# Performance work log

Hardware: AMD Instinct MI355X
Metric: run time of the kernel (lower is better)

## Reference

```python
import jax, jax.numpy as jnp
import numpy as np

N_NODES = 100000
N_REL = 8
N_EDGES = 1_600_000
ED = 64   # entity_dim
RD = 64   # relation_dim
H = 4     # attention heads
A = 16    # attention dim per head
D1, D2 = 32, 16  # conv_dim_list


def _leaky(x):
    return jax.nn.leaky_relu(x, 0.01)  # nn.LeakyReLU default slope


def _l2norm(x):
    n = jnp.sqrt(jnp.sum(x * x, axis=1, keepdims=True))
    return x / jnp.maximum(n, 1e-12)  # F.normalize(p=2, dim=1)


def setup_inputs() -> dict:
    key = jax.random.key(0)
    ks = jax.random.split(key, 16)
    s = 0.1
    return dict(
        src=jax.random.randint(ks[0], (N_EDGES,), 0, N_NODES),
        dst=jax.random.randint(ks[1], (N_EDGES,), 0, N_NODES),
        etype=jax.random.randint(ks[2], (N_EDGES,), 0, N_REL),
        node_ids=jnp.arange(N_NODES),
        user_ids=jax.random.randint(ks[3], (1000,), 0, N_NODES),
        item_ids=jax.random.randint(ks[4], (4096,), 0, N_NODES),
        entity_embed=jax.random.normal(ks[5], (N_NODES, ED)) * s,
        rel_embed=jax.random.normal(ks[6], (N_REL, RD)) * s,
        W_R=jax.random.normal(ks[7], (N_REL, ED, RD)) * s,
        W_A=jax.random.normal(ks[8], (RD, H, A)) * s,
        W1_0=jax.random.normal(ks[9], (ED, D1 // H)) * s,
        b1_0=jnp.zeros((D1 // H,)),
        W2_0=jax.random.normal(ks[10], (ED, D1 // H)) * s,
        b2_0=jnp.zeros((D1 // H,)),
        W1_1=jax.random.normal(ks[11], (D1, D2 // H)) * s,
        b1_1=jnp.zeros((D2 // H,)),
        W2_1=jax.random.normal(ks[12], (D1, D2 // H)) * s,
        b2_1=jnp.zeros((D2 // H,)),
    )


def _compute_attention(entity_embed, rel_embed, W_R, W_A, src, dst, etype):
    # relation-specific edge attention: tanh(e_src W_r W_A) * tanh(e_dst W_r W_A + r W_A)
    WA_flat = W_A.reshape(RD, H * A)
    W_ra = jnp.einsum('rij,jk->rik', W_R, WA_flat)          # [R, ED, H*A]
    proj = jnp.einsum('ne,rek->rnk', entity_embed, W_ra)    # [R, N, H*A]
    r_emb_a = rel_embed @ WA_flat                           # [R, H*A]
    r_mul_t = jnp.tanh(proj[etype, src])                    # [E, H*A]
    r_mul_h = jnp.tanh(proj[etype, dst] + r_emb_a[etype])   # [E, H*A]
    att = (r_mul_t * r_mul_h).reshape(-1, H, A).sum(-1)     # [E, H]
    # edge softmax over incoming edges of each dst node, per head
    m = jax.ops.segment_max(att, dst, num_segments=N_NODES)
    m = jnp.where(jnp.isfinite(m), m, 0.0)
    e = jnp.exp(att - m[dst])
    z = jax.ops.segment_sum(e, dst, num_segments=N_NODES)
    return e / jnp.maximum(z[dst], 1e-12)                   # [E, H]


def _bi_layer(ego, att, src, dst, W1, b1, W2, b2, out_dim):
    # u_mul_e + sum: message = node[src] (broadcast over heads) * att[:, :, None]
    in_dim = ego.shape[1]
    msg = ego[src][:, None, :] * att[:, :, None]            # [E, H, in]
    N_h = jax.ops.segment_sum(msg, dst, num_segments=N_NODES)  # [N, H, in]
    node = ego[:, None, :]                                  # [N, 1, in]
    out1 = _leaky((node + N_h).reshape(-1, in_dim) @ W1 + b1).reshape(N_NODES, out_dim)
    out2 = _leaky((node * N_h).reshape(-1, in_dim) @ W2 + b2).reshape(N_NODES, out_dim)
    return out1 + out2  # dropout p=0 (eval)


def reference(src, dst, etype, node_ids, user_ids, item_ids,
              entity_embed, rel_embed, W_R, W_A,
              W1_0, b1_0, W2_0, b2_0, W1_1, b1_1, W2_1, b2_1):
    att = _compute_attention(entity_embed, rel_embed, W_R, W_A, src, dst, etype)
    ego = entity_embed[node_ids]
    ego1 = _bi_layer(ego, att, src, dst, W1_0, b1_0, W2_0, b2_0, D1)
    ego2 = _bi_layer(ego1, att, src, dst, W1_1, b1_1, W2_1, b2_1, D2)
    all_embed = jnp.concatenate([ego, _l2norm(ego1), _l2norm(ego2)], axis=1)  # [N, 112]
    return all_embed[user_ids] @ all_embed[item_ids].T     # [1000, 4096]
```

## Files before the change

kernel.cpp:

```cpp
#include <hip/hip_runtime.h>
#include <hip/hip_bf16.h>
#include <math.h>

#define NN 100000
#define NR 8
#define NE 1600000

typedef __attribute__((ext_vector_type(8))) short short8v;
typedef __attribute__((ext_vector_type(4))) float float4v;
typedef __attribute__((ext_vector_type(2))) float float2v;

__device__ inline float bf2f(unsigned short u) {
  union { unsigned int i; float f; } v; v.i = ((unsigned int)u) << 16; return v.f;
}
__device__ inline unsigned short f2bf(float f) {
  __hip_bfloat16 h = __float2bfloat16(f);
  return *reinterpret_cast<unsigned short*>(&h);
}
__device__ inline float fast_tanh(float x) {
  float ex = __expf(2.f * x);
  return 1.f - 2.f * __builtin_amdgcn_rcpf(ex + 1.f);
}
__device__ inline unsigned char f2fp8(float f) {
  unsigned int p = __builtin_amdgcn_cvt_pk_fp8_f32(f, f, 0, false);
  return (unsigned char)(p & 0xff);
}

__global__ void k_prep(const float* __restrict__ W_R, const float* __restrict__ W_A,
                       const float* __restrict__ rel, unsigned short* __restrict__ Wbf,
                       float* __restrict__ r_emb_a) {
  int tid = blockIdx.x * 256 + threadIdx.x;
  if (tid < NR * 64 * 64) {
    int r = tid >> 12;
    int i = (tid >> 6) & 63;
    int k = tid & 63;
    float acc = 0.f;
    const float* wr = W_R + (r * 64 + i) * 64;
    for (int j = 0; j < 64; ++j) acc += wr[j] * W_A[j * 64 + k];
    Wbf[(r * 64 + k) * 64 + i] = f2bf(acc);
  } else if (tid < NR * 64 * 64 + NR * 64) {
    int idx = tid - NR * 64 * 64;
    int r = idx >> 6, k = idx & 63;
    float acc = 0.f;
    for (int j = 0; j < 64; ++j) acc += rel[r * 64 + j] * W_A[j * 64 + k];
    r_emb_a[idx] = acc;
  }
}

__global__ void k_cvt(const float* __restrict__ E, unsigned short* __restrict__ Ebf) {
  int i = blockIdx.x * 256 + threadIdx.x;
  float4 v = ((const float4*)E)[i];
  ushort4 o;
  o.x = f2bf(v.x); o.y = f2bf(v.y); o.z = f2bf(v.z); o.w = f2bf(v.w);
  ((ushort4*)Ebf)[i] = o;
}

__global__ void k_proj(const unsigned short* __restrict__ Ebf,
                       const unsigned short* __restrict__ Wbf,
                       const float* __restrict__ rea,
                       unsigned char* __restrict__ T1, unsigned char* __restrict__ T2) {
  int wv = threadIdx.x >> 6, lane = threadIdx.x & 63;
  int n0 = blockIdx.x * 64 + wv * 16;
  int mrow = lane & 15, kg = lane >> 4;
  int nodeA = n0 + mrow;
  if (nodeA >= NN) nodeA = NN - 1;
  const short8v a0 = *(const short8v*)(Ebf + (long)nodeA * 64 + kg * 8);
  const short8v a1 = *(const short8v*)(Ebf + (long)nodeA * 64 + 32 + kg * 8);
  int orow = kg * 4;
  for (int ct = 0; ct < 32; ++ct) {
    int c = ct * 16 + mrow;
    const short8v b0 = *(const short8v*)(Wbf + c * 64 + kg * 8);
    const short8v b1 = *(const short8v*)(Wbf + c * 64 + 32 + kg * 8);
    float4v acc = {0.f, 0.f, 0.f, 0.f};
    acc = __builtin_amdgcn_mfma_f32_16x16x32_bf16(a0, b0, acc, 0, 0, 0);
    acc = __builtin_amdgcn_mfma_f32_16x16x32_bf16(a1, b1, acc, 0, 0, 0);
    float rv = rea[c];
    int r = c >> 6, kk = c & 63;
#pragma unroll
    for (int i = 0; i < 4; ++i) {
      int nd = n0 + orow + i;
      if (nd < NN) {
        long base = ((long)r * NN + nd) * 64 + kk;
        T1[base] = f2fp8(fast_tanh(acc[i]));
        T2[base] = f2fp8(fast_tanh(acc[i] + rv));
      }
    }
  }
}

__global__ void k_hist(const int* __restrict__ dst, int* __restrict__ cnt) {
  int e = blockIdx.x * 256 + threadIdx.x;
  if (e < NE) atomicAdd(&cnt[dst[e]], 1);
}

#define SCAN_B 1024
#define NSCAN ((NN + SCAN_B - 1) / SCAN_B)

__global__ void k_scan1(const int* __restrict__ cnt, int* __restrict__ rowp,
                        int* __restrict__ bsum) {
  __shared__ int s[SCAN_B];
  int t = threadIdx.x, g = blockIdx.x * SCAN_B + t;
  s[t] = (g < NN) ? cnt[g] : 0;
  __syncthreads();
  for (int off = 1; off < SCAN_B; off <<= 1) {
    int x = (t >= off) ? s[t - off] : 0;
    __syncthreads();
    s[t] += x;
    __syncthreads();
  }
  if (g < NN) rowp[g + 1] = s[t];
  if (t == SCAN_B - 1) bsum[blockIdx.x] = s[t];
}

__global__ void k_scan2(int* bsum) {
  if (threadIdx.x == 0) {
    int acc = 0;
    for (int i = 0; i < NSCAN; ++i) { int v = bsum[i]; bsum[i] = acc; acc += v; }
  }
}

__global__ void k_scan3(int* rowp, const int* __restrict__ bsum) {
  int t = threadIdx.x, g = blockIdx.x * SCAN_B + t;
  if (g < NN) rowp[g + 1] += bsum[blockIdx.x];
  if (g == 0) rowp[0] = 0;
}

__global__ void k_scatter(const int* __restrict__ src, const int* __restrict__ dst,
                          const int* __restrict__ etype, const int* __restrict__ rowp,
                          int* __restrict__ cur, int* __restrict__ srcs,
                          int* __restrict__ ets, int* __restrict__ dsts) {
  int e = blockIdx.x * 256 + threadIdx.x;
  if (e >= NE) return;
  int d = dst[e];
  int p = rowp[d] + atomicAdd(&cur[d], 1);
  srcs[p] = src[e];
  ets[p] = etype[e];
  dsts[p] = d;
}

__global__ void k_att(const unsigned char* __restrict__ T1,
                      const unsigned char* __restrict__ T2,
                      const int* __restrict__ srcs, const int* __restrict__ dsts,
                      const int* __restrict__ ets, float* __restrict__ att) {
  int gid = blockIdx.x * 256 + threadIdx.x;
  int e = gid >> 2;
  int h = gid & 3;
  if (e >= NE) return;
  int r = ets[e], s = srcs[e], d = dsts[e];
  const uint4 av = *(const uint4*)(T1 + ((long)r * NN + s) * 64 + h * 16);
  const uint4 bv = *(const uint4*)(T2 + ((long)r * NN + d) * 64 + h * 16);
  const unsigned int* ap = (const unsigned int*)&av;
  const unsigned int* bp = (const unsigned int*)&bv;
  float acc = 0.f;
#pragma unroll
  for (int i = 0; i < 4; ++i) {
    float2v a0 = __builtin_amdgcn_cvt_pk_f32_fp8(ap[i], false);
    float2v a1 = __builtin_amdgcn_cvt_pk_f32_fp8(ap[i], true);
    float2v b0 = __builtin_amdgcn_cvt_pk_f32_fp8(bp[i], false);
    float2v b1 = __builtin_amdgcn_cvt_pk_f32_fp8(bp[i], true);
    acc += a0.x * b0.x + a0.y * b0.y + a1.x * b1.x + a1.y * b1.y;
  }
  att[e * 4 + h] = acc;
}

__global__ void k_nodemax(const int* __restrict__ rowp, const float* __restrict__ att,
                          float* __restrict__ minv) {
  int gid = blockIdx.x * 256 + threadIdx.x;
  int n = gid >> 2, h = gid & 3;
  if (n >= NN) return;
  int p0 = rowp[n], p1 = rowp[n + 1];
  float m = -3.4e38f;
  for (int p = p0; p < p1; ++p) m = fmaxf(m, att[p * 4 + h]);
  float z = 0.f;
  for (int p = p0; p < p1; ++p) z += __expf(att[p * 4 + h] - m);
  minv[n * 8 + h] = m;
  minv[n * 8 + 4 + h] = 1.f / fmaxf(z, 1e-12f);
}

__global__ void k_attn(const float* __restrict__ att, const float* __restrict__ minv,
                       const int* __restrict__ dsts, float* __restrict__ attn) {
  int gid = blockIdx.x * 256 + threadIdx.x;
  int e = gid >> 2, h = gid & 3;
  if (e >= NE) return;
  int d = dsts[e];
  attn[gid] = __expf(att[gid] - minv[d * 8 + h]) * minv[d * 8 + 4 + h];
}

__global__ void k_fused0(const float* __restrict__ E, const unsigned short* __restrict__ Ebf,
                         const float* __restrict__ attn,
                         const int* __restrict__ rowp, const int* __restrict__ srcs,
                         const float* __restrict__ W1, const float* __restrict__ b1,
                         const float* __restrict__ W2, const float* __restrict__ b2,
                         float* __restrict__ ego1, unsigned short* __restrict__ ego1bf) {
  __shared__ float wt1[8][68], wt2[8][68];
  __shared__ float bb[16];
  __shared__ float s1[4][4][68], s2[4][4][68];
  int t = threadIdx.x;
  for (int i = t; i < 512; i += 256) {
    int d = i >> 3, j = i & 7;
    wt1[j][d] = W1[i];
    wt2[j][d] = W2[i];
  }
  if (t < 8) bb[t] = b1[t];
  else if (t < 16) bb[t] = b2[t - 8];
  __syncthreads();
  int wv = t >> 6, lane = t & 63;
  int n = blockIdx.x * 4 + wv;
  int p0 = rowp[n], p1 = rowp[n + 1];
  int g = lane >> 4, q = lane & 15;
  float acc[4][4];
#pragma unroll
  for (int h = 0; h < 4; ++h)
#pragma unroll
    for (int j = 0; j < 4; ++j) acc[h][j] = 0.f;
  for (int p = p0 + g; p < p1; p += 4) {
    int s = srcs[p];
    float4 a = ((const float4*)attn)[p];
    ushort4 ev = *(const ushort4*)(Ebf + s * 64 + q * 4);
    float e0 = bf2f(ev.x), e1 = bf2f(ev.y), e2 = bf2f(ev.z), e3 = bf2f(ev.w);
    acc[0][0] += a.x * e0; acc[0][1] += a.x * e1; acc[0][2] += a.x * e2; acc[0][3] += a.x * e3;
    acc[1][0] += a.y * e0; acc[1][1] += a.y * e1; acc[1][2] += a.y * e2; acc[1][3] += a.y * e3;
    acc[2][0] += a.z * e0; acc[2][1] += a.z * e1; acc[2][2] += a.z * e2; acc[2][3] += a.z * e3;
    acc[3][0] += a.w * e0; acc[3][1] += a.w * e1; acc[3][2] += a.w * e2; acc[3][3] += a.w * e3;
  }
#pragma unroll
  for (int h = 0; h < 4; ++h)
#pragma unroll
    for (int j = 0; j < 4; ++j) {
      acc[h][j] += __shfl_xor(acc[h][j], 16);
      acc[h][j] += __shfl_xor(acc[h][j], 32);
    }
  if (lane < 16) {
    float4 edv = *(const float4*)(E + n * 64 + q * 4);
#pragma unroll
    for (int h = 0; h < 4; ++h) {
      float4 v1, v2;
      v1.x = edv.x + acc[h][0]; v2.x = edv.x * acc[h][0];
      v1.y = edv.y + acc[h][1]; v2.y = edv.y * acc[h][1];
      v1.z = edv.z + acc[h][2]; v2.z = edv.z * acc[h][2];
      v1.w = edv.w + acc[h][3]; v2.w = edv.w * acc[h][3];
      *(float4*)&s1[wv][h][q * 4] = v1;
      *(float4*)&s2[wv][h][q * 4] = v2;
    }
  }
  __syncthreads();
  int h = (lane >> 3) & 3, j = lane & 7;
  const float* sp = (lane < 32) ? &s1[wv][h][0] : &s2[wv][h][0];
  const float* wp = (lane < 32) ? &wt1[j][0] : &wt2[j][0];
  float o = 0.f;
#pragma unroll
  for (int d = 0; d < 64; d += 4) {
    float4 sv = *(const float4*)(sp + d);
    float4 wv4 = *(const float4*)(wp + d);
    o += sv.x * wv4.x + sv.y * wv4.y + sv.z * wv4.z + sv.w * wv4.w;
  }
  o += (lane < 32) ? bb[j] : bb[8 + j];
  o = (o >= 0.f) ? o : 0.01f * o;
  float other = __shfl_xor(o, 32);
  if (lane < 32) {
    float r = o + other;
    ego1[n * 32 + h * 8 + j] = r;
    ego1bf[n * 32 + h * 8 + j] = f2bf(r);
  }
}

__global__ void k_fused1(const float* __restrict__ ego1, const unsigned short* __restrict__ E1bf,
                         const float* __restrict__ attn,
                         const int* __restrict__ rowp, const int* __restrict__ srcs,
                         const float* __restrict__ W1, const float* __restrict__ b1,
                         const float* __restrict__ W2, const float* __restrict__ b2,
                         float* __restrict__ ego2) {
  __shared__ float wt1[4][36], wt2[4][36], bb[8];
  __shared__ float s1[4][4][36], s2[4][4][36];
  int t = threadIdx.x;
  if (t < 128) { int d = t >> 2, j = t & 3; wt1[j][d] = W1[t]; wt2[j][d] = W2[t]; }
  if (t < 4) bb[t] = b1[t];
  else if (t < 8) bb[t] = b2[t - 4];
  __syncthreads();
  int wv = t >> 6, lane = t & 63;
  int n = blockIdx.x * 4 + wv;
  int p0 = rowp[n], p1 = rowp[n + 1];
  int g = lane >> 3, q = lane & 7;
  float acc[4][4];
#pragma unroll
  for (int h = 0; h < 4; ++h)
#pragma unroll
    for (int j = 0; j < 4; ++j) acc[h][j] = 0.f;
  for (int p = p0 + g; p < p1; p += 8) {
    int s = srcs[p];
    float4 a = ((const float4*)attn)[p];
    ushort4 ev = *(const ushort4*)(E1bf + s * 32 + q * 4);
    float e0 = bf2f(ev.x), e1 = bf2f(ev.y), e2 = bf2f(ev.z), e3 = bf2f(ev.w);
    acc[0][0] += a.x * e0; acc[0][1] += a.x * e1; acc[0][2] += a.x * e2; acc[0][3] += a.x * e3;
    acc[1][0] += a.y * e0; acc[1][1] += a.y * e1; acc[1][2] += a.y * e2; acc[1][3] += a.y * e3;
    acc[2][0] += a.z * e0; acc[2][1] += a.z * e1; acc[2][2] += a.z * e2; acc[2][3] += a.z * e3;
    acc[3][0] += a.w * e0; acc[3][1] += a.w * e1; acc[3][2] += a.w * e2; acc[3][3] += a.w * e3;
  }
#pragma unroll
  for (int h = 0; h < 4; ++h)
#pragma unroll
    for (int j = 0; j < 4; ++j) {
      acc[h][j] += __shfl_xor(acc[h][j], 8);
      acc[h][j] += __shfl_xor(acc[h][j], 16);
      acc[h][j] += __shfl_xor(acc[h][j], 32);
    }
  if (lane < 8) {
    float4 e1v = *(const float4*)(ego1 + n * 32 + q * 4);
#pragma unroll
    for (int h = 0; h < 4; ++h) {
      float4 v1, v2;
      v1.x = e1v.x + acc[h][0]; v2.x = e1v.x * acc[h][0];
      v1.y = e1v.y + acc[h][1]; v2.y = e1v.y * acc[h][1];
      v1.z = e1v.z + acc[h][2]; v2.z = e1v.z * acc[h][2];
      v1.w = e1v.w + acc[h][3]; v2.w = e1v.w * acc[h][3];
      *(float4*)&s1[wv][h][q * 4] = v1;
      *(float4*)&s2[wv][h][q * 4] = v2;
    }
  }
  __syncthreads();
  if (lane < 32) {
    int h = (lane >> 2) & 3, j = lane & 3;
    const float* sp = (lane < 16) ? &s1[wv][h][0] : &s2[wv][h][0];
    const float* wp = (lane < 16) ? &wt1[j][0] : &wt2[j][0];
    float o = 0.f;
#pragma unroll
    for (int d = 0; d < 32; d += 4) {
      float4 sv = *(const float4*)(sp + d);
      float4 wv4 = *(const float4*)(wp + d);
      o += sv.x * wv4.x + sv.y * wv4.y + sv.z * wv4.z + sv.w * wv4.w;
    }
    o += (lane < 16) ? bb[j] : bb[4 + j];
    o = (o >= 0.f) ? o : 0.01f * o;
    float other = __shfl_xor(o, 16);
    if (lane < 16) ego2[n * 16 + h * 4 + j] = o + other;
  }
}

__global__ void k_uv(const float* __restrict__ E, const float* __restrict__ E1,
                     const float* __restrict__ E2, const int* __restrict__ uid,
                     const int* __restrict__ iid, float* __restrict__ U,
                     float* __restrict__ V) {
  int row = (blockIdx.x * 256 + threadIdx.x) >> 6;
  int lane = threadIdx.x & 63;
  if (row >= 1000 + 4096) return;
  int id = (row < 1000) ? uid[row] : iid[row - 1000];
  float* dest = (row < 1000) ? (U + row * 112) : (V + (row - 1000) * 112);
  float v1 = (lane < 32) ? E1[id * 32 + lane] : 0.f;
  float s1 = v1 * v1;
  for (int m = 1; m < 64; m <<= 1) s1 += __shfl_xor(s1, m);
  float v2 = (lane < 16) ? E2[id * 16 + lane] : 0.f;
  float s2 = v2 * v2;
  for (int m = 1; m < 64; m <<= 1) s2 += __shfl_xor(s2, m);
  float i1 = 1.f / fmaxf(sqrtf(s1), 1e-12f);
  float i2 = 1.f / fmaxf(sqrtf(s2), 1e-12f);
  dest[lane] = E[id * 64 + lane];
  if (lane < 32) dest[64 + lane] = v1 * i1;
  if (lane < 16) dest[96 + lane] = v2 * i2;
}

__global__ void k_gemm(const float* __restrict__ U, const float* __restrict__ V,
                       float* __restrict__ C) {
  __shared__ float Us[16][113], Vs[16][113];
  int tx = threadIdx.x & 15, ty = threadIdx.x >> 4;
  int u0 = blockIdx.y * 16, v0 = blockIdx.x * 16;
  for (int i = threadIdx.x; i < 16 * 112; i += 256) {
    int rr = i / 112, cc = i % 112;
    int ur = u0 + rr;
    Us[rr][cc] = (ur < 1000) ? U[ur * 112 + cc] : 0.f;
    Vs[rr][cc] = V[(v0 + rr) * 112 + cc];
  }
  __syncthreads();
  int u = u0 + ty;
  if (u >= 1000) return;
  float acc = 0.f;
#pragma unroll
  for (int k = 0; k < 112; ++k) acc += Us[ty][k] * Vs[tx][k];
  C[u * 4096 + v0 + tx] = acc;
}

extern "C" void kernel_launch(void* const* d_in, const int* in_sizes, int n_in,
                              void* d_out, int out_size, void* d_ws, size_t ws_size,
                              hipStream_t stream) {
  const int* src = (const int*)d_in[0];
  const int* dst = (const int*)d_in[1];
  const int* etype = (const int*)d_in[2];
  const int* uid = (const int*)d_in[4];
  const int* iid = (const int*)d_in[5];
  const float* entity = (const float*)d_in[6];
  const float* rel = (const float*)d_in[7];
  const float* W_R = (const float*)d_in[8];
  const float* W_A = (const float*)d_in[9];
  const float* W1_0 = (const float*)d_in[10];
  const float* b1_0 = (const float*)d_in[11];
  const float* W2_0 = (const float*)d_in[12];
  const float* b2_0 = (const float*)d_in[13];
  const float* W1_1 = (const float*)d_in[14];
  const float* b1_1 = (const float*)d_in[15];
  const float* W2_1 = (const float*)d_in[16];
  const float* b2_1 = (const float*)d_in[17];
  float* out = (float*)d_out;

  char* ws = (char*)d_ws;
  unsigned char*  T1   = (unsigned char*) (ws + 0);
  float*          ego1 = (float*)         (ws + 0);
  unsigned short* e1bf = (unsigned short*)(ws + 12800000);
  float*          ego2 = (float*)         (ws + 19200000);
  float*          U    = (float*)         (ws + 25600000);
  float*          V    = (float*)         (ws + 26048000);
  unsigned char*  T2   = (unsigned char*) (ws + 51200000);
  float*          attn = (float*)         (ws + 51200000);
  float*          att  = (float*)         (ws + 102400000);
  int*            srcs = (int*)           (ws + 128000000);
  int*            ets  = (int*)           (ws + 134400000);
  int*            dsts = (int*)           (ws + 140800000);
  int*            rowp = (int*)           (ws + 147200000);
  int*            cnt  = (int*)           (ws + 147600128);
  int*            bsum = (int*)           (ws + 148000256);
  unsigned short* Wbf  = (unsigned short*)(ws + 148000768);
  float*          rea  = (float*)         (ws + 148066304);
  unsigned short* Ebf  = (unsigned short*)(ws + 148068352);
  float*          minv = (float*)         (ws + 160868352);

  hipMemsetAsync(cnt, 0, NN * sizeof(int), stream);
  k_prep<<<130, 256, 0, stream>>>(W_R, W_A, rel, Wbf, rea);
  k_cvt<<<6250, 256, 0, stream>>>(entity, Ebf);
  k_proj<<<(NN + 63) / 64, 256, 0, stream>>>(Ebf, Wbf, rea, T1, T2);
  k_hist<<<NE / 256, 256, 0, stream>>>(dst, cnt);
  k_scan1<<<NSCAN, SCAN_B, 0, stream>>>(cnt, rowp, bsum);
  k_scan2<<<1, 64, 0, stream>>>(bsum);
  k_scan3<<<NSCAN, SCAN_B, 0, stream>>>(rowp, bsum);
  hipMemsetAsync(cnt, 0, NN * sizeof(int), stream);
  k_scatter<<<NE / 256, 256, 0, stream>>>(src, dst, etype, rowp, cnt, srcs, ets, dsts);
  k_att<<<NE * 4 / 256, 256, 0, stream>>>(T1, T2, srcs, dsts, ets, att);
  k_nodemax<<<(NN * 4 + 255) / 256, 256, 0, stream>>>(rowp, att, minv);
  k_attn<<<NE * 4 / 256, 256, 0, stream>>>(att, minv, dsts, attn);
  k_fused0<<<NN / 4, 256, 0, stream>>>(entity, Ebf, attn, rowp, srcs,
                                       W1_0, b1_0, W2_0, b2_0, ego1, e1bf);
  k_fused1<<<NN / 4, 256, 0, stream>>>(ego1, e1bf, attn, rowp, srcs,
                                       W1_1, b1_1, W2_1, b2_1, ego2);
  k_uv<<<(1000 + 4096 + 3) / 4, 256, 0, stream>>>(entity, ego1, ego2, uid, iid, U, V);
  k_gemm<<<dim3(4096 / 16, (1000 + 15) / 16), 256, 0, stream>>>(U, V, out);
}
```

Measured before the change: 593.0 us.

## Pack edge records and fuse edge softmax into one wave-per-node kernel

The scatter now writes one packed 8-byte record per edge (src<<3|etype, dst) in place of three separate int arrays, and k_att writes the src array itself for the later layers. The node-max and normalize kernels are replaced by one softmax kernel that gives each node a 64-lane wave, reduces max and sum with shuffles over contiguous CSR attention, and normalizes in place. This cuts a launch, the minv buffer and the per-edge dst gather, and the wave-per-node layout gives coalesced reads. The cost is idle lanes on low-degree nodes (about 16 edges per node on average) and three passes over the attention array within the kernel.

```diff
diff --git a/kernel.cpp b/kernel.cpp
--- a/kernel.cpp
+++ b/kernel.cpp
@@ -127,26 +127,29 @@
 
 __global__ void k_scatter(const int* __restrict__ src, const int* __restrict__ dst,
                           const int* __restrict__ etype, const int* __restrict__ rowp,
-                          int* __restrict__ cur, int* __restrict__ srcs,
-                          int* __restrict__ ets, int* __restrict__ dsts) {
+                          int* __restrict__ cur, uint2* __restrict__ rec) {
   int e = blockIdx.x * 256 + threadIdx.x;
   if (e >= NE) return;
   int d = dst[e];
   int p = rowp[d] + atomicAdd(&cur[d], 1);
-  srcs[p] = src[e];
-  ets[p] = etype[e];
-  dsts[p] = d;
+  uint2 rv;
+  rv.x = ((unsigned int)src[e] << 3) | (unsigned int)etype[e];
+  rv.y = (unsigned int)d;
+  rec[p] = rv;
 }
 
 __global__ void k_att(const unsigned char* __restrict__ T1,
                       const unsigned char* __restrict__ T2,
-                      const int* __restrict__ srcs, const int* __restrict__ dsts,
-                      const int* __restrict__ ets, float* __restrict__ att) {
+                      const uint2* __restrict__ rec, int* __restrict__ srcs,
+                      float* __restrict__ att) {
   int gid = blockIdx.x * 256 + threadIdx.x;
   int e = gid >> 2;
   int h = gid & 3;
   if (e >= NE) return;
-  int r = ets[e], s = srcs[e], d = dsts[e];
+  uint2 rv = rec[e];
+  int r = rv.x & 7;
+  int s = rv.x >> 3;
+  int d = (int)rv.y;
   const uint4 av = *(const uint4*)(T1 + ((long)r * NN + s) * 64 + h * 16);
   const uint4 bv = *(const uint4*)(T2 + ((long)r * NN + d) * 64 + h * 16);
   const unsigned int* ap = (const unsigned int*)&av;
@@ -160,30 +163,29 @@
     float2v b1 = __builtin_amdgcn_cvt_pk_f32_fp8(bp[i], true);
     acc += a0.x * b0.x + a0.y * b0.y + a1.x * b1.x + a1.y * b1.y;
   }
-  att[e * 4 + h] = acc;
-}
-
-__global__ void k_nodemax(const int* __restrict__ rowp, const float* __restrict__ att,
-                          float* __restrict__ minv) {
-  int gid = blockIdx.x * 256 + threadIdx.x;
-  int n = gid >> 2, h = gid & 3;
+  att[gid] = acc;
+  if (h == 0) srcs[e] = s;
+}
+
+__global__ void k_softmax(const int* __restrict__ rowp, float* __restrict__ att) {
+  int n = (blockIdx.x * 256 + threadIdx.x) >> 6;
+  int lane = threadIdx.x & 63;
   if (n >= NN) return;
-  int p0 = rowp[n], p1 = rowp[n + 1];
+  int i0 = rowp[n] * 4, i1 = rowp[n + 1] * 4;
   float m = -3.4e38f;
-  for (int p = p0; p < p1; ++p) m = fmaxf(m, att[p * 4 + h]);
+  for (int i = i0 + lane; i < i1; i += 64) m = fmaxf(m, att[i]);
+  m = fmaxf(m, __shfl_xor(m, 4));
+  m = fmaxf(m, __shfl_xor(m, 8));
+  m = fmaxf(m, __shfl_xor(m, 16));
+  m = fmaxf(m, __shfl_xor(m, 32));
   float z = 0.f;
-  for (int p = p0; p < p1; ++p) z += __expf(att[p * 4 + h] - m);
-  minv[n * 8 + h] = m;
-  minv[n * 8 + 4 + h] = 1.f / fmaxf(z, 1e-12f);
-}
-
-__global__ void k_attn(const float* __restrict__ att, const float* __restrict__ minv,
-                       const int* __restrict__ dsts, float* __restrict__ attn) {
-  int gid = blockIdx.x * 256 + threadIdx.x;
-  int e = gid >> 2, h = gid & 3;
-  if (e >= NE) return;
-  int d = dsts[e];
-  attn[gid] = __expf(att[gid] - minv[d * 8 + h]) * minv[d * 8 + 4 + h];
+  for (int i = i0 + lane; i < i1; i += 64) z += __expf(att[i] - m);
+  z += __shfl_xor(z, 4);
+  z += __shfl_xor(z, 8);
+  z += __shfl_xor(z, 16);
+  z += __shfl_xor(z, 32);
+  float inv = 1.f / fmaxf(z, 1e-12f);
+  for (int i = i0 + lane; i < i1; i += 64) att[i] = __expf(att[i] - m) * inv;
 }
 
 __global__ void k_fused0(const float* __restrict__ E, const unsigned short* __restrict__ Ebf,
@@ -408,18 +410,15 @@
   float*          U    = (float*)         (ws + 25600000);
   float*          V    = (float*)         (ws + 26048000);
   unsigned char*  T2   = (unsigned char*) (ws + 51200000);
-  float*          attn = (float*)         (ws + 51200000);
   float*          att  = (float*)         (ws + 102400000);
-  int*            srcs = (int*)           (ws + 128000000);
-  int*            ets  = (int*)           (ws + 134400000);
-  int*            dsts = (int*)           (ws + 140800000);
+  uint2*          rec  = (uint2*)         (ws + 128000000);
+  int*            srcs = (int*)           (ws + 140800000);
   int*            rowp = (int*)           (ws + 147200000);
   int*            cnt  = (int*)           (ws + 147600128);
   int*            bsum = (int*)           (ws + 148000256);
   unsigned short* Wbf  = (unsigned short*)(ws + 148000768);
   float*          rea  = (float*)         (ws + 148066304);
   unsigned short* Ebf  = (unsigned short*)(ws + 148068352);
-  float*          minv = (float*)         (ws + 160868352);
 
   hipMemsetAsync(cnt, 0, NN * sizeof(int), stream);
   k_prep<<<130, 256, 0, stream>>>(W_R, W_A, rel, Wbf, rea);
@@ -430,13 +429,12 @@
   k_scan2<<<1, 64, 0, stream>>>(bsum);
   k_scan3<<<NSCAN, SCAN_B, 0, stream>>>(rowp, bsum);
   hipMemsetAsync(cnt, 0, NN * sizeof(int), stream);
-  k_scatter<<<NE / 256, 256, 0, stream>>>(src, dst, etype, rowp, cnt, srcs, ets, dsts);
-  k_att<<<NE * 4 / 256, 256, 0, stream>>>(T1, T2, srcs, dsts, ets, att);
-  k_nodemax<<<(NN * 4 + 255) / 256, 256, 0, stream>>>(rowp, att, minv);
-  k_attn<<<NE * 4 / 256, 256, 0, stream>>>(att, minv, dsts, attn);
-  k_fused0<<<NN / 4, 256, 0, stream>>>(entity, Ebf, attn, rowp, srcs,
+  k_scatter<<<NE / 256, 256, 0, stream>>>(src, dst, etype, rowp, cnt, rec);
+  k_att<<<NE * 4 / 256, 256, 0, stream>>>(T1, T2, rec, srcs, att);
+  k_softmax<<<NN / 4, 256, 0, stream>>>(rowp, att);
+  k_fused0<<<NN / 4, 256, 0, stream>>>(entity, Ebf, att, rowp, srcs,
                                        W1_0, b1_0, W2_0, b2_0, ego1, e1bf);
-  k_fused1<<<NN / 4, 256, 0, stream>>>(ego1, e1bf, attn, rowp, srcs,
+  k_fused1<<<NN / 4, 256, 0, stream>>>(ego1, e1bf, att, rowp, srcs,
                                        W1_1, b1_1, W2_1, b2_1, ego2);
   k_uv<<<(1000 + 4096 + 3) / 4, 256, 0, stream>>>(entity, ego1, ego2, uid, iid, U, V);
   k_gemm<<<dim3(4096 / 16, (1000 + 15) / 16), 256, 0, stream>>>(U, V, out);
```

Measured after the change: 610.2 us. 2.9% more time.
